# Performance work log

Measured on AMD Instinct MI355X. Metric: run time of the kernel, lower is better.

## Reference

```python
import jax, jax.numpy as jnp
import numpy as np

B, H, W, C_IN, C_QK = 8, 64, 64, 256, 32


def setup_inputs() -> dict:
    key = jax.random.key(0)
    ks = jax.random.split(key, 5)
    x = jax.random.normal(ks[0], (B, H, W, C_IN), dtype=jnp.float32)
    Wq = jax.random.normal(ks[1], (C_IN, C_QK), dtype=jnp.float32) * 0.05
    bq = jnp.zeros((C_QK,), dtype=jnp.float32)
    Wk = jax.random.normal(ks[2], (C_IN, C_QK), dtype=jnp.float32) * 0.05
    bk = jnp.zeros((C_QK,), dtype=jnp.float32)
    Wv = jax.random.normal(ks[3], (C_IN, C_IN), dtype=jnp.float32) * 0.05
    bv = jnp.zeros((C_IN,), dtype=jnp.float32)
    gamma = jax.random.normal(ks[4], (1,), dtype=jnp.float32)
    return {"x": x, "Wq": Wq, "bq": bq, "Wk": Wk, "bk": bk, "Wv": Wv, "bv": bv, "gamma": gamma}


def reference(x, Wq, bq, Wk, bk, Wv, bv, gamma):
    b, h, w, c_in = x.shape
    n = h * w
    xt = x.reshape(b, n, c_in)                      # tokens: (B, N, C_in)
    # 1x1 convs == per-token channel matmuls
    q = xt @ Wq + bq                                # (B, N, Cqk)
    k = xt @ Wk + bk                                # (B, N, Cqk)
    v = xt @ Wv + bv                                # (B, N, C_in)
    energy = jnp.einsum('bnc,bmc->bnm', q, k)       # (B, N, N)
    attn = jax.nn.softmax(energy, axis=-1)
    # original: out = (V^T @ A^T)^T == A @ V
    out = jnp.einsum('bnm,bmc->bnc', attn, v)       # (B, N, C_in)
    out = out.reshape(b, h, w, c_in)
    out = gamma * out + x                           # residual with learned scale
    return jnp.mean(out, axis=-1)                   # channel-mean pool -> (B, H, W)
```

## Files before the change

kernel.cpp:

```cpp
#include <hip/hip_runtime.h>
#include <hip/hip_bf16.h>


typedef _Float16 half8  __attribute__((ext_vector_type(8)));
typedef _Float16 half4v __attribute__((ext_vector_type(4)));
typedef float    f32x4  __attribute__((ext_vector_type(4)));

#define LOG2E 1.4426950408889634f

#if __has_builtin(__builtin_amdgcn_exp2f)
#define EXP2(x) __builtin_amdgcn_exp2f(x)
#else
#define EXP2(x) exp2f(x)
#endif

__global__ __launch_bounds__(256) void prep_kernel(
    const float* __restrict__ Wq, const float* __restrict__ Wk,
    const float* __restrict__ Wv, const float* __restrict__ bv,
    _Float16* __restrict__ Wfr, float* __restrict__ wvbar, float* __restrict__ bvbar)
{
  int bid = blockIdx.x, tid = threadIdx.x;
  if (bid < 64) {
    int col = bid, c = tid;
    float v = (col < 32) ? Wq[c * 32 + col] : Wk[c * 32 + (col - 32)];
    int ch = c >> 5, quad = (c >> 3) & 3, j = c & 7;
    Wfr[(size_t)((ch * 4 + quad) * 64 + col) * 8 + j] = (_Float16)v;
  } else if (bid < 128) {
    int row = (bid - 64) * 4 + (tid >> 6);
    int lane = tid & 63;
    const float* p = Wv + (size_t)row * 256 + lane * 4;
    float s = p[0] + p[1] + p[2] + p[3];
    #pragma unroll
    for (int off = 32; off >= 1; off >>= 1) s += __shfl_xor(s, off);
    if (lane == 0) wvbar[row] = s * (1.0f / 256.0f);
  } else {
    if (tid < 64) {
      const float* p = bv + tid * 4;
      float s = p[0] + p[1] + p[2] + p[3];
      #pragma unroll
      for (int off = 32; off >= 1; off >>= 1) s += __shfl_xor(s, off);
      if (tid == 0) bvbar[0] = s * (1.0f / 256.0f);
    }
  }
}

__global__ __launch_bounds__(256) void proj_kernel(
    const float* __restrict__ x, const _Float16* __restrict__ Wfr,
    const float* __restrict__ bq, const float* __restrict__ bk,
    const float* __restrict__ wvbar, const float* __restrict__ bvbar,
    _Float16* __restrict__ Qh, _Float16* __restrict__ Kh,
    float* __restrict__ vbarO, float* __restrict__ xbarO)
{
  __shared__ _Float16 XT[64 * 264];
  int tid = threadIdx.x, blk = blockIdx.x;
  size_t tok0 = (size_t)blk * 64;

  const float4* xg4 = (const float4*)x;
  #pragma unroll
  for (int i = 0; i < 16; ++i) {
    int f = i * 256 + tid;
    int tok = f >> 6, c4 = f & 63;
    float4 v = xg4[(size_t)blk * 4096 + f];
    half4v h;
    h.x = (_Float16)v.x; h.y = (_Float16)v.y; h.z = (_Float16)v.z; h.w = (_Float16)v.w;
    *(half4v*)&XT[tok * 264 + c4 * 4] = h;
  }
  __syncthreads();

  if (tid < 64) {
    float vs = 0.f, xs = 0.f;
    #pragma unroll 4
    for (int g = 0; g < 32; ++g) {
      half8 h = *(const half8*)&XT[tid * 264 + g * 8];
      #pragma unroll
      for (int j = 0; j < 8; ++j) {
        float xv = (float)h[j];
        vs += xv * wvbar[g * 8 + j];
        xs += xv;
      }
    }
    vbarO[tok0 + tid] = vs + bvbar[0];
    xbarO[tok0 + tid] = xs * (1.0f / 256.0f);
  }

  int lane = tid & 63, w = tid >> 6;
  int l15 = lane & 15, quad = lane >> 4;
  f32x4 acc[4] = {(f32x4){0,0,0,0},(f32x4){0,0,0,0},(f32x4){0,0,0,0},(f32x4){0,0,0,0}};
  #pragma unroll
  for (int ch = 0; ch < 8; ++ch) {
    half8 a = *(const half8*)&XT[(w * 16 + l15) * 264 + ch * 32 + quad * 8];
    #pragma unroll
    for (int ct = 0; ct < 4; ++ct) {
      half8 bf = *(const half8*)(Wfr + (size_t)((ch * 4 + quad) * 64 + ct * 16 + l15) * 8);
      acc[ct] = __builtin_amdgcn_mfma_f32_16x16x32_f16(a, bf, acc[ct], 0, 0, 0);
    }
  }
  #pragma unroll
  for (int ct = 0; ct < 4; ++ct) {
    int col = ct * 16 + l15;
    #pragma unroll
    for (int r = 0; r < 4; ++r) {
      int token = w * 16 + quad * 4 + r;
      if (ct < 2) {
        float val = (acc[ct][r] + bq[col]) * LOG2E;
        Qh[(tok0 + token) * 32 + col] = (_Float16)val;
      } else {
        float val = acc[ct][r] + bk[col - 32];
        Kh[(tok0 + token) * 32 + (col - 32)] = (_Float16)val;
      }
    }
  }
}

__global__ __launch_bounds__(512, 4) void flash_kernel(
    const _Float16* __restrict__ Qh, const _Float16* __restrict__ Kh,
    const float* __restrict__ vbar, const float* __restrict__ xbar,
    const float* __restrict__ gamma, float* __restrict__ out)
{
  __shared__ float Lp[8][64];
  __shared__ float Op[8][64];
  int tid = threadIdx.x, blk = blockIdx.x;
  int b = blk >> 6, qt = blk & 63;
  int lane = tid & 63, w = tid >> 6;
  int l15 = lane & 15, quad = lane >> 4;

  const _Float16* Qb = Qh + (size_t)b * 4096 * 32;
  const _Float16* Kb = Kh + (size_t)b * 4096 * 32;
  const float* vb = vbar + (size_t)b * 4096;

  half8 aq[4];
  #pragma unroll
  for (int af = 0; af < 4; ++af)
    aq[af] = *(const half8*)(Qb + (size_t)(qt * 64 + af * 16 + l15) * 32 + quad * 8);

  float lacc[4][4], oacc[4][4];
  #pragma unroll
  for (int af = 0; af < 4; ++af)
    #pragma unroll
    for (int r = 0; r < 4; ++r) { lacc[af][r] = 0.f; oacc[af][r] = 0.f; }
  const f32x4 cinit = {-88.f, -88.f, -88.f, -88.f};

  const _Float16* kfrag = Kb + ((size_t)w * 512 + l15) * 32 + quad * 8;
  const float* vfrag = vb + w * 512 + l15;

  #pragma unroll 2
  for (int kt = 0; kt < 8; ++kt) {
    half8 bk8[4];
    float vbl[4];
    #pragma unroll
    for (int ct = 0; ct < 4; ++ct) {
      bk8[ct] = *(const half8*)(kfrag + (size_t)(kt * 64 + ct * 16) * 32);
      vbl[ct] = vfrag[kt * 64 + ct * 16];
    }
    #pragma unroll
    for (int af = 0; af < 4; ++af) {
      f32x4 sc[4];
      #pragma unroll
      for (int ct = 0; ct < 4; ++ct)
        sc[ct] = __builtin_amdgcn_mfma_f32_16x16x32_f16(aq[af], bk8[ct], cinit, 0, 0, 0);
      #pragma unroll
      for (int r = 0; r < 4; ++r) {
        float p0 = EXP2(sc[0][r]), p1 = EXP2(sc[1][r]);
        float p2 = EXP2(sc[2][r]), p3 = EXP2(sc[3][r]);
        lacc[af][r] += (p0 + p1) + (p2 + p3);
        oacc[af][r] += ((p0 * vbl[0] + p1 * vbl[1]) + (p2 * vbl[2] + p3 * vbl[3]));
      }
    }
  }

  #pragma unroll
  for (int af = 0; af < 4; ++af)
    #pragma unroll
    for (int r = 0; r < 4; ++r) {
      #pragma unroll
      for (int off = 1; off < 16; off <<= 1) {
        lacc[af][r] += __shfl_xor(lacc[af][r], off);
        oacc[af][r] += __shfl_xor(oacc[af][r], off);
      }
    }

  if (l15 == 0) {
    #pragma unroll
    for (int af = 0; af < 4; ++af)
      #pragma unroll
      for (int r = 0; r < 4; ++r) {
        Lp[w][af * 16 + quad * 4 + r] = lacc[af][r];
        Op[w][af * 16 + quad * 4 + r] = oacc[af][r];
      }
  }
  __syncthreads();
  if (tid < 64) {
    float l = ((Lp[0][tid] + Lp[1][tid]) + (Lp[2][tid] + Lp[3][tid]))
            + ((Lp[4][tid] + Lp[5][tid]) + (Lp[6][tid] + Lp[7][tid]));
    float o = ((Op[0][tid] + Op[1][tid]) + (Op[2][tid] + Op[3][tid]))
            + ((Op[4][tid] + Op[5][tid]) + (Op[6][tid] + Op[7][tid]));
    size_t g = (size_t)b * 4096 + qt * 64 + tid;
    out[g] = gamma[0] * (o / l) + xbar[g];
  }
}

extern "C" void kernel_launch(void* const* d_in, const int* in_sizes, int n_in,
                              void* d_out, int out_size, void* d_ws, size_t ws_size,
                              hipStream_t stream)
{
  const float* x     = (const float*)d_in[0];
  const float* Wq    = (const float*)d_in[1];
  const float* bq    = (const float*)d_in[2];
  const float* Wk    = (const float*)d_in[3];
  const float* bk    = (const float*)d_in[4];
  const float* Wv    = (const float*)d_in[5];
  const float* bv    = (const float*)d_in[6];
  const float* gamma = (const float*)d_in[7];
  float* out = (float*)d_out;

  char* ws = (char*)d_ws;
  _Float16* Wfr  = (_Float16*)(ws);
  float* wvbar   = (float*)(ws + 32768);
  float* bvbar   = (float*)(ws + 33792);
  _Float16* Qh   = (_Float16*)(ws + 65536);
  _Float16* Kh   = (_Float16*)(ws + 65536 + 2097152);
  float* vbarA   = (float*)(ws + 65536 + 4194304);
  float* xbarA   = (float*)(ws + 65536 + 4194304 + 131072);

  prep_kernel<<<129, 256, 0, stream>>>(Wq, Wk, Wv, bv, Wfr, wvbar, bvbar);
  proj_kernel<<<512, 256, 0, stream>>>(x, Wfr, bq, bk, wvbar, bvbar, Qh, Kh, vbarA, xbarA);
  flash_kernel<<<512, 512, 0, stream>>>(Qh, Kh, vbarA, xbarA, gamma, out);
}
```

Baseline: 112.5 us.

## Halve projection tile to 32 tokens and spread row reductions across all threads

The projection kernel now handles 32 tokens per block and launches twice as many blocks. Each wave computes two column tiles for one 16-token group, so the MFMA work is split differently across the four waves. The per-token v-bar and x-bar reductions now use all 256 threads (8 per token) with shuffle reductions, where before only 64 threads did serial loops. The aim is more parallelism and occupancy for the memory-bound x read, at the cost of reading the Wfr fragments once per smaller tile.

```diff
diff --git a/kernel.cpp b/kernel.cpp
--- a/kernel.cpp
+++ b/kernel.cpp
@@ -44,68 +44,80 @@
   }
 }
 
-__global__ __launch_bounds__(256) void proj_kernel(
+__global__ __launch_bounds__(256, 4) void proj_kernel(
     const float* __restrict__ x, const _Float16* __restrict__ Wfr,
     const float* __restrict__ bq, const float* __restrict__ bk,
     const float* __restrict__ wvbar, const float* __restrict__ bvbar,
     _Float16* __restrict__ Qh, _Float16* __restrict__ Kh,
     float* __restrict__ vbarO, float* __restrict__ xbarO)
 {
-  __shared__ _Float16 XT[64 * 264];
+  __shared__ _Float16 XT[32 * 264];
   int tid = threadIdx.x, blk = blockIdx.x;
-  size_t tok0 = (size_t)blk * 64;
+  size_t tok0 = (size_t)blk * 32;
 
   const float4* xg4 = (const float4*)x;
   #pragma unroll
-  for (int i = 0; i < 16; ++i) {
+  for (int i = 0; i < 8; ++i) {
     int f = i * 256 + tid;
     int tok = f >> 6, c4 = f & 63;
-    float4 v = xg4[(size_t)blk * 4096 + f];
+    float4 v = xg4[(size_t)blk * 2048 + f];
     half4v h;
     h.x = (_Float16)v.x; h.y = (_Float16)v.y; h.z = (_Float16)v.z; h.w = (_Float16)v.w;
     *(half4v*)&XT[tok * 264 + c4 * 4] = h;
   }
   __syncthreads();
 
-  if (tid < 64) {
+  {
+    int tok = tid >> 3, t8 = tid & 7;
     float vs = 0.f, xs = 0.f;
-    #pragma unroll 4
-    for (int g = 0; g < 32; ++g) {
-      half8 h = *(const half8*)&XT[tid * 264 + g * 8];
-      #pragma unroll
-      for (int j = 0; j < 8; ++j) {
-        float xv = (float)h[j];
-        vs += xv * wvbar[g * 8 + j];
-        xs += xv;
-      }
-    }
-    vbarO[tok0 + tid] = vs + bvbar[0];
-    xbarO[tok0 + tid] = xs * (1.0f / 256.0f);
+    const float4* wv4 = (const float4*)(wvbar + t8 * 32);
+    #pragma unroll
+    for (int g = 0; g < 4; ++g) {
+      half8 h = *(const half8*)&XT[tok * 264 + t8 * 32 + g * 8];
+      float4 wa = wv4[g * 2], wb = wv4[g * 2 + 1];
+      float x0 = (float)h[0], x1 = (float)h[1], x2 = (float)h[2], x3 = (float)h[3];
+      float x4 = (float)h[4], x5 = (float)h[5], x6 = (float)h[6], x7 = (float)h[7];
+      vs += ((x0 * wa.x + x1 * wa.y) + (x2 * wa.z + x3 * wa.w))
+          + ((x4 * wb.x + x5 * wb.y) + (x6 * wb.z + x7 * wb.w));
+      xs += ((x0 + x1) + (x2 + x3)) + ((x4 + x5) + (x6 + x7));
+    }
+    #pragma unroll
+    for (int off = 1; off < 8; off <<= 1) {
+      vs += __shfl_xor(vs, off);
+      xs += __shfl_xor(xs, off);
+    }
+    if (t8 == 0) {
+      vbarO[tok0 + tok] = vs + bvbar[0];
+      xbarO[tok0 + tok] = xs * (1.0f / 256.0f);
+    }
   }
 
   int lane = tid & 63, w = tid >> 6;
   int l15 = lane & 15, quad = lane >> 4;
-  f32x4 acc[4] = {(f32x4){0,0,0,0},(f32x4){0,0,0,0},(f32x4){0,0,0,0},(f32x4){0,0,0,0}};
+  int tg = w & 1, ctb = (w >> 1) * 2;
+  f32x4 acc[2] = {(f32x4){0,0,0,0},(f32x4){0,0,0,0}};
   #pragma unroll
   for (int ch = 0; ch < 8; ++ch) {
-    half8 a = *(const half8*)&XT[(w * 16 + l15) * 264 + ch * 32 + quad * 8];
-    #pragma unroll
-    for (int ct = 0; ct < 4; ++ct) {
+    half8 a = *(const half8*)&XT[(tg * 16 + l15) * 264 + ch * 32 + quad * 8];
+    #pragma unroll
+    for (int cti = 0; cti < 2; ++cti) {
+      int ct = ctb + cti;
       half8 bf = *(const half8*)(Wfr + (size_t)((ch * 4 + quad) * 64 + ct * 16 + l15) * 8);
-      acc[ct] = __builtin_amdgcn_mfma_f32_16x16x32_f16(a, bf, acc[ct], 0, 0, 0);
-    }
-  }
-  #pragma unroll
-  for (int ct = 0; ct < 4; ++ct) {
+      acc[cti] = __builtin_amdgcn_mfma_f32_16x16x32_f16(a, bf, acc[cti], 0, 0, 0);
+    }
+  }
+  #pragma unroll
+  for (int cti = 0; cti < 2; ++cti) {
+    int ct = ctb + cti;
     int col = ct * 16 + l15;
     #pragma unroll
     for (int r = 0; r < 4; ++r) {
-      int token = w * 16 + quad * 4 + r;
+      int token = tg * 16 + quad * 4 + r;
       if (ct < 2) {
-        float val = (acc[ct][r] + bq[col]) * LOG2E;
+        float val = (acc[cti][r] + bq[col]) * LOG2E;
         Qh[(tok0 + token) * 32 + col] = (_Float16)val;
       } else {
-        float val = acc[ct][r] + bk[col - 32];
+        float val = acc[cti][r] + bk[col - 32];
         Kh[(tok0 + token) * 32 + (col - 32)] = (_Float16)val;
       }
     }
@@ -223,6 +235,6 @@
   float* xbarA   = (float*)(ws + 65536 + 4194304 + 131072);
 
   prep_kernel<<<129, 256, 0, stream>>>(Wq, Wk, Wv, bv, Wfr, wvbar, bvbar);
-  proj_kernel<<<512, 256, 0, stream>>>(x, Wfr, bq, bk, wvbar, bvbar, Qh, Kh, vbarA, xbarA);
+  proj_kernel<<<1024, 256, 0, stream>>>(x, Wfr, bq, bk, wvbar, bvbar, Qh, Kh, vbarA, xbarA);
   flash_kernel<<<512, 512, 0, stream>>>(Qh, Kh, vbarA, xbarA, gamma, out);
 }
```

Measured after the change: 113.7 us. Within noise of the previous version (+1.0%).
